# Optimization experiments

Measured on AMD Instinct MI355X. Metric: run time of the kernel, lower is better.

The kernel has to match this reference:

```python
import jax, jax.numpy as jnp
import numpy as np

CODEBOOK_SIZE = 256
EMBED_DIM = 32
N_TOKENS = 524288
EPS = 1e-6


def l2norm(t, eps=EPS):
    # F.normalize(p=2): x / max(||x||, eps)
    n = jnp.sqrt(jnp.sum(t * t, axis=-1, keepdims=True))
    return t / jnp.maximum(n, eps)


def setup_inputs() -> dict:
    key = jax.random.key(0)
    kx, kw = jax.random.split(key)
    x = jax.random.normal(kx, (N_TOKENS, EMBED_DIM), dtype=jnp.float32)
    # embedding.weight.data.uniform_(-1/codebook_size, 1/codebook_size)
    codebook = jax.random.uniform(
        kw, (CODEBOOK_SIZE, EMBED_DIM), dtype=jnp.float32,
        minval=-1.0 / CODEBOOK_SIZE, maxval=1.0 / CODEBOOK_SIZE)
    return {"x": x, "codebook": codebook}


def reference(x, codebook):
    # --- find_nearest_codes: cdist + argmin + gather ---
    # squared euclidean distances have the same argmin as torch.cdist
    x2 = jnp.sum(x * x, axis=-1, keepdims=True)            # [N, 1]
    c2 = jnp.sum(codebook * codebook, axis=-1)             # [K]
    d2 = x2 - 2.0 * (x @ codebook.T) + c2[None, :]         # [N, K]
    indices = jnp.argmin(d2, axis=1)                       # [N] int
    quantized = codebook[indices]                          # [N, D]

    # --- update_usage: histogram over codes ---
    counts = jnp.zeros((CODEBOOK_SIZE,), dtype=jnp.float32).at[indices].add(1.0)

    # --- rotate_to(x, quantized): rotation-trick gradient estimator ---
    u = jax.lax.stop_gradient(l2norm(x))                   # detached direction of src
    q = jax.lax.stop_gradient(l2norm(quantized))           # detached direction of tgt
    w = jax.lax.stop_gradient(l2norm(u + q))               # Householder bisector, detached
    e = x                                                  # gradient flows through e only
    ew = jnp.sum(e * w, axis=-1, keepdims=True)            # (e @ w_col)
    eu = jnp.sum(e * u, axis=-1, keepdims=True)            # (e @ u_col)
    rotated = e - 2.0 * ew * w + 2.0 * eu * q              # [N, D]

    return rotated, indices, counts
```

## Files before the change

### kernel.cpp

```cpp
#include <hip/hip_runtime.h>

#define N_TOK   524288
#define KC      256
#define D       32
#define EPSF    1e-6f
#define TPT     64
#define NTILES  (N_TOK / TPT)
#define NBLK    768
#define BLKT    256

__global__ __launch_bounds__(BLKT) void vq_main(
    const float* __restrict__ x, const float* __restrict__ cb,
    float* __restrict__ out_rot, float* __restrict__ out_idx,
    float* __restrict__ ws_hist, float* __restrict__ out_cnt, int use_ws)
{
    __shared__ float ct[D][KC];
    __shared__ float c2s[KC];
    __shared__ float xt[D][TPT];
    __shared__ float x2s[TPT];
    __shared__ int   bidx[TPT];
    __shared__ float hist[KC];

    const int tid = threadIdx.x;

    {
#pragma clang fp contract(off)
        const float4* cb4 = (const float4*)(cb + (size_t)tid * D);
        float4 r[8];
#pragma unroll
        for (int j = 0; j < 8; j++) r[j] = cb4[j];
        float t[32];
#pragma unroll
        for (int j = 0; j < 8; j++) {
            t[4 * j + 0] = r[j].x * r[j].x;
            t[4 * j + 1] = r[j].y * r[j].y;
            t[4 * j + 2] = r[j].z * r[j].z;
            t[4 * j + 3] = r[j].w * r[j].w;
        }
        float pr[8];
#pragma unroll
        for (int j = 0; j < 8; j++)
            pr[j] = ((t[j] + t[j + 8]) + t[j + 16]) + t[j + 24];
        c2s[tid] = ((pr[0] + pr[1]) + (pr[2] + pr[3])) + ((pr[4] + pr[5]) + (pr[6] + pr[7]));
#pragma unroll
        for (int j = 0; j < 8; j++) {
            ct[4 * j + 0][tid] = r[j].x;
            ct[4 * j + 1][tid] = r[j].y;
            ct[4 * j + 2][tid] = r[j].z;
            ct[4 * j + 3][tid] = r[j].w;
        }
        hist[tid] = 0.f;
    }
    const int tt = tid >> 4;
    const int tc = tid & 15;
    __syncthreads();

    for (int tile = blockIdx.x; tile < NTILES; tile += gridDim.x) {
        const int tok0 = tile * TPT;

        {
            const float4* xg = (const float4*)(x + (size_t)tok0 * D + (size_t)tid * 8);
            float4 a = xg[0], b = xg[1];
            int tok = tid >> 2;
            int k0  = (tid & 3) * 8;
            xt[k0 + 0][tok] = a.x; xt[k0 + 1][tok] = a.y;
            xt[k0 + 2][tok] = a.z; xt[k0 + 3][tok] = a.w;
            xt[k0 + 4][tok] = b.x; xt[k0 + 5][tok] = b.y;
            xt[k0 + 6][tok] = b.z; xt[k0 + 7][tok] = b.w;
        }
        __syncthreads();

        if (tid < TPT) {
#pragma clang fp contract(off)
            float t[32];
#pragma unroll
            for (int k = 0; k < 32; k++) { float v = xt[k][tid]; t[k] = v * v; }
            float pr[8];
#pragma unroll
            for (int j = 0; j < 8; j++)
                pr[j] = ((t[j] + t[j + 8]) + t[j + 16]) + t[j + 24];
            x2s[tid] = ((pr[0] + pr[1]) + (pr[2] + pr[3])) + ((pr[4] + pr[5]) + (pr[6] + pr[7]));
        }
        __syncthreads();

        float x4[4];
#pragma unroll
        for (int i = 0; i < 4; i++) x4[i] = x2s[tt * 4 + i];

        float bestv[4] = {3.4e38f, 3.4e38f, 3.4e38f, 3.4e38f};
        int   besti[4] = {0x7fffffff, 0x7fffffff, 0x7fffffff, 0x7fffffff};
#pragma unroll
        for (int chunk = 0; chunk < 2; chunk++) {
            const int cbase = chunk * 128 + tc * 8;
            float acc[4][8];
#pragma unroll
            for (int i = 0; i < 4; i++)
#pragma unroll
                for (int j = 0; j < 8; j++) acc[i][j] = 0.f;

#pragma unroll 8
            for (int k = 0; k < D; k++) {
                const float4 xv = *(const float4*)&xt[k][tt * 4];
                const float4 c0 = *(const float4*)&ct[k][cbase];
                const float4 c1 = *(const float4*)&ct[k][cbase + 4];
                const float xs[4] = {xv.x, xv.y, xv.z, xv.w};
                const float cs[8] = {c0.x, c0.y, c0.z, c0.w, c1.x, c1.y, c1.z, c1.w};
#pragma unroll
                for (int i = 0; i < 4; i++)
#pragma unroll
                    for (int j = 0; j < 8; j++)
                        acc[i][j] = __builtin_fmaf(xs[i], cs[j], acc[i][j]);
            }
#pragma unroll
            for (int j = 0; j < 8; j++) {
                const float c2v = c2s[cbase + j];
#pragma unroll
                for (int i = 0; i < 4; i++) {
                    float t2 = x4[i] - 2.0f * acc[i][j];
                    float s  = t2 + c2v;
                    if (s < bestv[i]) { bestv[i] = s; besti[i] = cbase + j; }
                }
            }
        }
#pragma unroll
        for (int m = 1; m < 16; m <<= 1) {
#pragma unroll
            for (int i = 0; i < 4; i++) {
                float ov = __shfl_xor(bestv[i], m, 64);
                int   oi = __shfl_xor(besti[i], m, 64);
                if (ov < bestv[i] || (ov == bestv[i] && oi < besti[i])) {
                    bestv[i] = ov; besti[i] = oi;
                }
            }
        }
        if (tc == 0) {
#pragma unroll
            for (int i = 0; i < 4; i++) bidx[tt * 4 + i] = besti[i];
        }
        __syncthreads();

        {
            const int tok = tid >> 2;
            const int sub = tid & 3;
            const size_t gtok = (size_t)tok0 + tok;
            const float4* xg = (const float4*)(x + gtok * D + sub * 8);
            float4 xa = xg[0], xb = xg[1];
            const int bi = bidx[tok];
            const float4* cg = (const float4*)(cb + (size_t)bi * D + sub * 8);
            float4 ca = cg[0], cbv = cg[1];

            float xs8[8] = {xa.x, xa.y, xa.z, xa.w, xb.x, xb.y, xb.z, xb.w};
            float cs8[8] = {ca.x, ca.y, ca.z, ca.w, cbv.x, cbv.y, cbv.z, cbv.w};

            float px2 = 0.f, pc2 = 0.f;
#pragma unroll
            for (int j = 0; j < 8; j++) { px2 = fmaf(xs8[j], xs8[j], px2); pc2 = fmaf(cs8[j], cs8[j], pc2); }
            float x2 = px2 + __shfl_xor(px2, 1, 64); x2 += __shfl_xor(x2, 2, 64);
            float c2 = pc2 + __shfl_xor(pc2, 1, 64); c2 += __shfl_xor(c2, 2, 64);
            const float inx = 1.f / fmaxf(sqrtf(x2), EPSF);
            const float inc = 1.f / fmaxf(sqrtf(c2), EPSF);

            float us8[8], qs8[8], ws8[8];
            float pw2 = 0.f;
#pragma unroll
            for (int j = 0; j < 8; j++) {
                us8[j] = xs8[j] * inx;
                qs8[j] = cs8[j] * inc;
                ws8[j] = us8[j] + qs8[j];
                pw2 = fmaf(ws8[j], ws8[j], pw2);
            }
            float w2 = pw2 + __shfl_xor(pw2, 1, 64); w2 += __shfl_xor(w2, 2, 64);
            const float inw = 1.f / fmaxf(sqrtf(w2), EPSF);

            float pew = 0.f, peu = 0.f;
#pragma unroll
            for (int j = 0; j < 8; j++) {
                ws8[j] *= inw;
                pew = fmaf(xs8[j], ws8[j], pew);
                peu = fmaf(xs8[j], us8[j], peu);
            }
            float ew = pew + __shfl_xor(pew, 1, 64); ew += __shfl_xor(ew, 2, 64);
            float eu = peu + __shfl_xor(peu, 1, 64); eu += __shfl_xor(eu, 2, 64);

            float ro[8];
#pragma unroll
            for (int j = 0; j < 8; j++)
                ro[j] = xs8[j] - 2.f * ew * ws8[j] + 2.f * eu * qs8[j];

            float4* og = (float4*)(out_rot + gtok * D + sub * 8);
            og[0] = make_float4(ro[0], ro[1], ro[2], ro[3]);
            og[1] = make_float4(ro[4], ro[5], ro[6], ro[7]);

            if (sub == 0) {
                out_idx[gtok] = (float)bi;
                atomicAdd(&hist[bi], 1.f);
            }
        }
        __syncthreads();
    }

    if (use_ws) ws_hist[(size_t)blockIdx.x * KC + tid] = hist[tid];
    else        atomicAdd(&out_cnt[tid], hist[tid]);
}

__global__ __launch_bounds__(256) void vq_reduce(const float* __restrict__ ws,
                                                 float* __restrict__ out_cnt)
{
    const int c = blockIdx.x * 8 + (threadIdx.x >> 5);
    const int l = threadIdx.x & 31;
    float s = 0.f;
    for (int b = l; b < NBLK; b += 32) s += ws[(size_t)b * KC + c];
#pragma unroll
    for (int m = 1; m < 32; m <<= 1) s += __shfl_xor(s, m, 64);
    if (l == 0) out_cnt[c] = s;
}

extern "C" void kernel_launch(void* const* d_in, const int* in_sizes, int n_in,
                              void* d_out, int out_size, void* d_ws, size_t ws_size,
                              hipStream_t stream)
{
    const float* x  = (const float*)d_in[0];
    const float* cb = (const float*)d_in[1];
    float* out      = (float*)d_out;
    float* out_rot  = out;
    float* out_idx  = out + (size_t)N_TOK * D;
    float* out_cnt  = out_idx + N_TOK;

    const size_t ws_need = (size_t)NBLK * KC * sizeof(float);
    const int use_ws = (ws_size >= ws_need) ? 1 : 0;
    if (!use_ws) hipMemsetAsync(out_cnt, 0, KC * sizeof(float), stream);

    vq_main<<<NBLK, BLKT, 0, stream>>>(x, cb, out_rot, out_idx,
                                       (float*)d_ws, out_cnt, use_ws);
    if (use_ws) vq_reduce<<<32, 256, 0, stream>>>((const float*)d_ws, out_cnt);
}
```

Measured before the change: 245.5 us.

## Double token tile, widen register microtile, add atomic dynamic tile scheduling

Doubles the tokens per tile to 128, so each thread now computes an 8x8 register block of token-by-code dot products instead of 4x8. That roughly doubles compute per shared-memory load and halves the per-tile barrier overhead. Tiles are now handed out dynamically through a global atomic counter kept in the workspace, which needs an extra memset and one atomic per tile. The epilogue loops twice per tile, and the trailing barrier was removed in favour of the one at the top of the loop. The larger accumulator set raises register pressure and may lower occupancy.

```diff
diff --git a/kernel.cpp b/kernel.cpp
--- a/kernel.cpp
+++ b/kernel.cpp
@@ -4,15 +4,17 @@
 #define KC      256
 #define D       32
 #define EPSF    1e-6f
-#define TPT     64
+#define TPT     128
 #define NTILES  (N_TOK / TPT)
 #define NBLK    768
 #define BLKT    256
 
+#define WS_HIST_OFF 64
+
 __global__ __launch_bounds__(BLKT) void vq_main(
     const float* __restrict__ x, const float* __restrict__ cb,
     float* __restrict__ out_rot, float* __restrict__ out_idx,
-    float* __restrict__ ws_hist, float* __restrict__ out_cnt, int use_ws)
+    float* __restrict__ ws, float* __restrict__ out_cnt, int use_ws)
 {
     __shared__ float ct[D][KC];
     __shared__ float c2s[KC];
@@ -20,6 +22,7 @@
     __shared__ float x2s[TPT];
     __shared__ int   bidx[TPT];
     __shared__ float hist[KC];
+    __shared__ int   sh_tile;
 
     const int tid = threadIdx.x;
 
@@ -53,20 +56,29 @@
     }
     const int tt = tid >> 4;
     const int tc = tid & 15;
-    __syncthreads();
-
-    for (int tile = blockIdx.x; tile < NTILES; tile += gridDim.x) {
+
+    uint* tile_cnt = (uint*)ws;
+
+    for (int it = 0; ; it++) {
+        if (use_ws) { if (tid == 0) sh_tile = (int)atomicAdd(tile_cnt, 1u); }
+        __syncthreads();
+        const int tile = use_ws ? sh_tile : (blockIdx.x + it * (int)gridDim.x);
+        if (tile >= NTILES) break;
         const int tok0 = tile * TPT;
 
         {
-            const float4* xg = (const float4*)(x + (size_t)tok0 * D + (size_t)tid * 8);
-            float4 a = xg[0], b = xg[1];
-            int tok = tid >> 2;
-            int k0  = (tid & 3) * 8;
-            xt[k0 + 0][tok] = a.x; xt[k0 + 1][tok] = a.y;
-            xt[k0 + 2][tok] = a.z; xt[k0 + 3][tok] = a.w;
-            xt[k0 + 4][tok] = b.x; xt[k0 + 5][tok] = b.y;
-            xt[k0 + 6][tok] = b.z; xt[k0 + 7][tok] = b.w;
+            const float4* xg = (const float4*)(x + (size_t)tok0 * D + (size_t)tid * 16);
+            float4 a = xg[0], b = xg[1], c = xg[2], d = xg[3];
+            const int tok = tid >> 1;
+            const int k0  = (tid & 1) * 16;
+            xt[k0 +  0][tok] = a.x; xt[k0 +  1][tok] = a.y;
+            xt[k0 +  2][tok] = a.z; xt[k0 +  3][tok] = a.w;
+            xt[k0 +  4][tok] = b.x; xt[k0 +  5][tok] = b.y;
+            xt[k0 +  6][tok] = b.z; xt[k0 +  7][tok] = b.w;
+            xt[k0 +  8][tok] = c.x; xt[k0 +  9][tok] = c.y;
+            xt[k0 + 10][tok] = c.z; xt[k0 + 11][tok] = c.w;
+            xt[k0 + 12][tok] = d.x; xt[k0 + 13][tok] = d.y;
+            xt[k0 + 14][tok] = d.z; xt[k0 + 15][tok] = d.w;
         }
         __syncthreads();
 
@@ -83,49 +95,56 @@
         }
         __syncthreads();
 
-        float x4[4];
-#pragma unroll
-        for (int i = 0; i < 4; i++) x4[i] = x2s[tt * 4 + i];
-
-        float bestv[4] = {3.4e38f, 3.4e38f, 3.4e38f, 3.4e38f};
-        int   besti[4] = {0x7fffffff, 0x7fffffff, 0x7fffffff, 0x7fffffff};
+        float x8[8];
+#pragma unroll
+        for (int i = 0; i < 8; i++) x8[i] = x2s[tt * 8 + i];
+
+        float bestv[8];
+        int   besti[8];
+#pragma unroll
+        for (int i = 0; i < 8; i++) { bestv[i] = 3.4e38f; besti[i] = 0x7fffffff; }
+
 #pragma unroll
         for (int chunk = 0; chunk < 2; chunk++) {
-            const int cbase = chunk * 128 + tc * 8;
-            float acc[4][8];
-#pragma unroll
-            for (int i = 0; i < 4; i++)
+            const int cb0 = chunk * 128 + tc * 4;
+            float acc[8][8];
+#pragma unroll
+            for (int i = 0; i < 8; i++)
 #pragma unroll
                 for (int j = 0; j < 8; j++) acc[i][j] = 0.f;
 
 #pragma unroll 8
             for (int k = 0; k < D; k++) {
-                const float4 xv = *(const float4*)&xt[k][tt * 4];
-                const float4 c0 = *(const float4*)&ct[k][cbase];
-                const float4 c1 = *(const float4*)&ct[k][cbase + 4];
-                const float xs[4] = {xv.x, xv.y, xv.z, xv.w};
-                const float cs[8] = {c0.x, c0.y, c0.z, c0.w, c1.x, c1.y, c1.z, c1.w};
-#pragma unroll
-                for (int i = 0; i < 4; i++)
+                const float4 xv0 = *(const float4*)&xt[k][tt * 8];
+                const float4 xv1 = *(const float4*)&xt[k][tt * 8 + 4];
+                const float4 cv0 = *(const float4*)&ct[k][cb0];
+                const float4 cv1 = *(const float4*)&ct[k][cb0 + 64];
+                const float xs[8] = {xv0.x, xv0.y, xv0.z, xv0.w, xv1.x, xv1.y, xv1.z, xv1.w};
+                const float cs[8] = {cv0.x, cv0.y, cv0.z, cv0.w, cv1.x, cv1.y, cv1.z, cv1.w};
+#pragma unroll
+                for (int i = 0; i < 8; i++)
 #pragma unroll
                     for (int j = 0; j < 8; j++)
                         acc[i][j] = __builtin_fmaf(xs[i], cs[j], acc[i][j]);
             }
 #pragma unroll
             for (int j = 0; j < 8; j++) {
-                const float c2v = c2s[cbase + j];
-#pragma unroll
-                for (int i = 0; i < 4; i++) {
-                    float t2 = x4[i] - 2.0f * acc[i][j];
+                const int   cidx = cb0 + ((j < 4) ? j : (60 + j));
+                const float c2v  = c2s[cidx];
+#pragma unroll
+                for (int i = 0; i < 8; i++) {
+                    float t2 = x8[i] - 2.0f * acc[i][j];
                     float s  = t2 + c2v;
-                    if (s < bestv[i]) { bestv[i] = s; besti[i] = cbase + j; }
+                    if (s < bestv[i] || (s == bestv[i] && cidx < besti[i])) {
+                        bestv[i] = s; besti[i] = cidx;
+                    }
                 }
             }
         }
 #pragma unroll
         for (int m = 1; m < 16; m <<= 1) {
 #pragma unroll
-            for (int i = 0; i < 4; i++) {
+            for (int i = 0; i < 8; i++) {
                 float ov = __shfl_xor(bestv[i], m, 64);
                 int   oi = __shfl_xor(besti[i], m, 64);
                 if (ov < bestv[i] || (ov == bestv[i] && oi < besti[i])) {
@@ -135,12 +154,13 @@
         }
         if (tc == 0) {
 #pragma unroll
-            for (int i = 0; i < 4; i++) bidx[tt * 4 + i] = besti[i];
-        }
-        __syncthreads();
-
-        {
-            const int tok = tid >> 2;
+            for (int i = 0; i < 8; i++) bidx[tt * 8 + i] = besti[i];
+        }
+        __syncthreads();
+
+#pragma unroll
+        for (int h = 0; h < 2; h++) {
+            const int tok = h * 64 + (tid >> 2);
             const int sub = tid & 3;
             const size_t gtok = (size_t)tok0 + tok;
             const float4* xg = (const float4*)(x + gtok * D + sub * 8);
@@ -196,10 +216,9 @@
                 atomicAdd(&hist[bi], 1.f);
             }
         }
-        __syncthreads();
     }
 
-    if (use_ws) ws_hist[(size_t)blockIdx.x * KC + tid] = hist[tid];
+    if (use_ws) ws[WS_HIST_OFF + (size_t)blockIdx.x * KC + tid] = hist[tid];
     else        atomicAdd(&out_cnt[tid], hist[tid]);
 }
 
@@ -209,7 +228,7 @@
     const int c = blockIdx.x * 8 + (threadIdx.x >> 5);
     const int l = threadIdx.x & 31;
     float s = 0.f;
-    for (int b = l; b < NBLK; b += 32) s += ws[(size_t)b * KC + c];
+    for (int b = l; b < NBLK; b += 32) s += ws[WS_HIST_OFF + (size_t)b * KC + c];
 #pragma unroll
     for (int m = 1; m < 32; m <<= 1) s += __shfl_xor(s, m, 64);
     if (l == 0) out_cnt[c] = s;
@@ -226,9 +245,13 @@
     float* out_idx  = out + (size_t)N_TOK * D;
     float* out_cnt  = out_idx + N_TOK;
 
-    const size_t ws_need = (size_t)NBLK * KC * sizeof(float);
+    const size_t ws_need = (WS_HIST_OFF + (size_t)NBLK * KC) * sizeof(float);
     const int use_ws = (ws_size >= ws_need) ? 1 : 0;
-    if (!use_ws) hipMemsetAsync(out_cnt, 0, KC * sizeof(float), stream);
+    if (use_ws) {
+        hipMemsetAsync(d_ws, 0, WS_HIST_OFF * sizeof(float), stream);
+    } else {
+        hipMemsetAsync(out_cnt, 0, KC * sizeof(float), stream);
+    }
 
     vq_main<<<NBLK, BLKT, 0, stream>>>(x, cb, out_rot, out_idx,
                                        (float*)d_ws, out_cnt, use_ws);
```

Result: slower. 350.5 us (+42.8%).
